# Performance work log

Measured on AMD Instinct MI355X. Metric: run time of the kernel, lower is better.

The kernel has to match this reference:

```python
import jax, jax.numpy as jnp
import numpy as np
from jax import lax

B, T, I, H = 256, 1024, 200, 16


def setup_inputs() -> dict:
    key = jax.random.key(0)
    ks = jax.random.split(key, 11)
    s = 0.05  # small init scale for weights
    return {
        "x": jax.random.normal(ks[0], (B, T, I), dtype=jnp.float32),
        "h0": jax.random.normal(ks[1], (B, H), dtype=jnp.float32),
        "c0": jax.random.normal(ks[2], (B, H), dtype=jnp.float32),
        "W_ih": jax.random.normal(ks[3], (4 * H, I), dtype=jnp.float32) * s,
        "W_hh": jax.random.normal(ks[4], (4 * H, H), dtype=jnp.float32) * s,
        "b_ih": jax.random.normal(ks[5], (4 * H,), dtype=jnp.float32) * s,
        "b_hh": jax.random.normal(ks[6], (4 * H,), dtype=jnp.float32) * s,
        "W1": jax.random.normal(ks[7], (H, H), dtype=jnp.float32) * s,
        "b1": jax.random.normal(ks[8], (H,), dtype=jnp.float32) * s,
        "W2": jax.random.normal(ks[9], (1, H), dtype=jnp.float32) * s,
        "b2": jax.random.normal(ks[10], (1,), dtype=jnp.float32) * s,
    }


def reference(x, h0, c0, W_ih, W_hh, b_ih, b_hh, W1, b1, W2, b2):
    # Precompute input projection for all timesteps: [B, T, 4H]
    x_proj = jnp.einsum("bti,gi->btg", x, W_ih) + b_ih + b_hh

    def step(carry, xt):  # xt: [B, 4H]
        h, c = carry
        gates = xt + h @ W_hh.T
        i, f, g, o = jnp.split(gates, 4, axis=-1)  # PyTorch gate order i,f,g,o
        i = jax.nn.sigmoid(i)
        f = jax.nn.sigmoid(f)
        g = jnp.tanh(g)
        o = jax.nn.sigmoid(o)
        c = f * c + i * g
        h = o * jnp.tanh(c)
        return (h, c), h

    _, hs = lax.scan(step, (h0, c0), x_proj.transpose(1, 0, 2))  # hs: [T, B, H]
    out = hs.transpose(1, 0, 2)  # [B, T, H]
    out = jax.nn.relu(out @ W1.T + b1)          # [B, T, H]
    out = jax.nn.sigmoid(out @ W2.T + b2)       # [B, T, 1]
    return jnp.mean(out, axis=1)                # [B, 1]
```

## Files before the change

kernel.cpp:

```cpp
#include <hip/hip_runtime.h>


#define T_LEN 1024
#define NB    256
#define CHUNK 128
#define NCH   (T_LEN / CHUNK)
#define XSTR  68

#define F2I(x) __float_as_int(x)
#define I2F(x) __int_as_float(x)
#define DPPF(v, ctrl) I2F(__builtin_amdgcn_update_dpp(F2I(v), F2I(v), (ctrl), 0xF, 0xF, false))
#define ROWSHL4(v) I2F(__builtin_amdgcn_update_dpp(F2I(v), F2I(v), 0x104, 0xF, 0xF, false))
#define RDLANE_I(v, l) __builtin_amdgcn_readlane((v), (l))

#define LOG2E 1.442695040888963f

typedef __bf16 bf16_t;
typedef bf16_t bf16x8 __attribute__((ext_vector_type(8)));
typedef float f32x4 __attribute__((ext_vector_type(4)));
typedef __fp16 half2_t __attribute__((ext_vector_type(2)));

#if __has_builtin(__builtin_amdgcn_exp2f)
__device__ __forceinline__ float fexp2(float x) { return __builtin_amdgcn_exp2f(x); }
#else
__device__ __forceinline__ float fexp2(float x) { return exp2f(x); }
#endif
#if __has_builtin(__builtin_amdgcn_rcpf)
__device__ __forceinline__ float frcp(float x) { return __builtin_amdgcn_rcpf(x); }
#else
__device__ __forceinline__ float frcp(float x) { return __fdividef(1.f, x); }
#endif

__device__ __forceinline__ half2_t i2h2(int x) { union { int i; half2_t h; } u; u.i = x; return u.h; }
__device__ __forceinline__ int h22i(half2_t h) { union { int i; half2_t h; } u; u.h = h; return u.i; }

#if __has_builtin(__builtin_amdgcn_fdot2)
#define FDOT2(a, b, c) __builtin_amdgcn_fdot2((a), (b), (c), false)
#else
__device__ __forceinline__ float FDOT2(half2_t a, half2_t b, float c) {
  return c + (float)a[0] * (float)b[0] + (float)a[1] * (float)b[1];
}
#endif

__device__ __forceinline__ float bf2f(unsigned short s) {
  return __uint_as_float(((unsigned int)s) << 16);
}
__device__ __forceinline__ unsigned int pkbf(float a, float b) {
  bf16_t x = (bf16_t)a, y = (bf16_t)b;
  unsigned short ux, uy;
  __builtin_memcpy(&ux, &x, 2); __builtin_memcpy(&uy, &y, 2);
  return (unsigned int)ux | ((unsigned int)uy << 16);
}

__global__ __launch_bounds__(256) void k0_prep(
    const float* __restrict__ Wih, const float* __restrict__ bih,
    const float* __restrict__ bhh, bf16x8* __restrict__ wB,
    float* __restrict__ biasPerm)
{
  const int idx = blockIdx.x * 256 + threadIdx.x;
  if (idx < 4 * 7 * 64) {
    const int f = idx / 448;
    const int rem = idx % 448;
    const int s = rem / 64;
    const int L = rem % 64;
    const int col = f * 16 + (L & 15);
    const int r = ((col & 3) << 4) | (col >> 2);
    const float sf = ((col & 3) == 2) ? (-2.f * LOG2E) : (-LOG2E);
    const int k0 = s * 32 + (L >> 4) * 8;
    bf16x8 v;
#pragma unroll
    for (int e = 0; e < 8; ++e) {
      const int k = k0 + e;
      const float w = (k < 200) ? (Wih[r * 200 + k] * sf) : 0.f;
      v[e] = (bf16_t)w;
    }
    wB[idx] = v;
  }
  if (blockIdx.x == 0 && threadIdx.x < 64) {
    const int c = threadIdx.x;
    const int r = ((c & 3) << 4) | (c >> 2);
    const float sf = ((c & 3) == 2) ? (-2.f * LOG2E) : (-LOG2E);
    biasPerm[c] = (bih[r] + bhh[r]) * sf;
  }
}

#define PACKH(hval, d0,d1,d2,d3,d4,d5,d6,d7) do {            \
    float _hn = ROWSHL4(hval);                               \
    int _pk = h22i(__builtin_amdgcn_cvt_pkrtz((hval), _hn)); \
    d0 = RDLANE_I(_pk,  0); d1 = RDLANE_I(_pk,  8);          \
    d2 = RDLANE_I(_pk, 16); d3 = RDLANE_I(_pk, 24);          \
    d4 = RDLANE_I(_pk, 32); d5 = RDLANE_I(_pk, 40);          \
    d6 = RDLANE_I(_pk, 48); d7 = RDLANE_I(_pk, 56);          \
  } while (0)

__global__ __launch_bounds__(256, 1) void mega(
    const float* __restrict__ x,
    const bf16x8* __restrict__ wB, const float* __restrict__ biasPerm,
    const float* __restrict__ h0, const float* __restrict__ c0,
    const float* __restrict__ Whh,
    unsigned short* __restrict__ hst)
{
  __shared__ float xsf[2][CHUNK * XSTR];

  const int tid  = threadIdx.x;
  const int lane = tid & 63;
  const int wid  = tid >> 6;
  const int b    = blockIdx.x;

  if (wid != 0) {
    const int pw   = wid - 1;
    const int L    = lane;
    const int mrow = L & 15;
    const int kg   = L >> 4;
    const int cb   = L & 15;

    bf16x8 Bv[28];
#pragma unroll
    for (int i = 0; i < 28; ++i) Bv[i] = wB[i * 64 + L];
    const float bv0 = biasPerm[ 0 + cb];
    const float bv1 = biasPerm[16 + cb];
    const float bv2 = biasPerm[32 + cb];
    const float bv3 = biasPerm[48 + cb];

    auto produce = [&](int pc) {
      for (int t8 = pw; t8 < 8; t8 += 3) {
        const int tile = pc * 8 + t8;
        const float* xr = x + ((size_t)b * T_LEN + tile * 16 + mrow) * 200;
        bf16x8 afr[7];
#pragma unroll
        for (int s = 0; s < 7; ++s) {
          const int k0 = s * 32 + kg * 8;
          bf16x8 v;
          if (k0 <= 192) {
            float4 a  = *reinterpret_cast<const float4*>(xr + k0);
            float4 b4 = *reinterpret_cast<const float4*>(xr + k0 + 4);
            v[0] = (bf16_t)a.x;  v[1] = (bf16_t)a.y;  v[2] = (bf16_t)a.z;  v[3] = (bf16_t)a.w;
            v[4] = (bf16_t)b4.x; v[5] = (bf16_t)b4.y; v[6] = (bf16_t)b4.z; v[7] = (bf16_t)b4.w;
          } else {
            v[0] = (bf16_t)0.f; v[1] = (bf16_t)0.f; v[2] = (bf16_t)0.f; v[3] = (bf16_t)0.f;
            v[4] = (bf16_t)0.f; v[5] = (bf16_t)0.f; v[6] = (bf16_t)0.f; v[7] = (bf16_t)0.f;
          }
          afr[s] = v;
        }

        f32x4 acc0 = {0.f,0.f,0.f,0.f}, acc1 = {0.f,0.f,0.f,0.f};
        f32x4 acc2 = {0.f,0.f,0.f,0.f}, acc3 = {0.f,0.f,0.f,0.f};
#pragma unroll
        for (int s = 0; s < 7; ++s) {
          acc0 = __builtin_amdgcn_mfma_f32_16x16x32_bf16(afr[s], Bv[0*7+s], acc0, 0,0,0);
          acc1 = __builtin_amdgcn_mfma_f32_16x16x32_bf16(afr[s], Bv[1*7+s], acc1, 0,0,0);
          acc2 = __builtin_amdgcn_mfma_f32_16x16x32_bf16(afr[s], Bv[2*7+s], acc2, 0,0,0);
          acc3 = __builtin_amdgcn_mfma_f32_16x16x32_bf16(afr[s], Bv[3*7+s], acc3, 0,0,0);
        }

        float* dst = xsf[pc & 1] + (t8 * 16) * XSTR;
#pragma unroll
        for (int q = 0; q < 4; ++q) {
          float* rowp = dst + (kg * 4 + q) * XSTR;
          rowp[ 0 + cb] = acc0[q] + bv0;
          rowp[16 + cb] = acc1[q] + bv1;
          rowp[32 + cb] = acc2[q] + bv2;
          rowp[48 + cb] = acc3[q] + bv3;
        }
      }
    };

    produce(0);
    for (int ch = 0; ch <= NCH; ++ch) {
      __syncthreads();
      if (ch + 1 < NCH) produce(ch + 1);
    }
    return;
  }

  __builtin_amdgcn_s_setprio(1);
  const int g = lane & 3;
  const int j = lane >> 2;
  const int r = (g << 4) | j;

  const float sfac = (g == 2) ? (-2.f * LOG2E) : (-LOG2E);
  const float pfac = (g == 0) ? (2.f * LOG2E) : ((g == 2) ? 2.f : 1.f);
  const float qfac = (g == 2) ? -1.f : 0.f;

  half2_t wpk[8];
#pragma unroll
  for (int q = 0; q < 4; ++q) {
    float4 w = *reinterpret_cast<const float4*>(Whh + r * 16 + q * 4);
    wpk[q * 2 + 0] = __builtin_amdgcn_cvt_pkrtz(w.x * sfac, w.y * sfac);
    wpk[q * 2 + 1] = __builtin_amdgcn_cvt_pkrtz(w.z * sfac, w.w * sfac);
  }

  float c = c0[b * 16 + j] * (2.f * LOG2E);
  float hmine = h0[b * 16 + j];
  int hp0, hp1, hp2, hp3, hp4, hp5, hp6, hp7;
  PACKH(hmine, hp0, hp1, hp2, hp3, hp4, hp5, hp6, hp7);

  unsigned short* hq = hst + (size_t)b * (16 * T_LEN) + j * T_LEN;

  __syncthreads();

  for (int ch = 0; ch < NCH; ++ch) {
    const float* xc = xsf[ch & 1];
    float buf[8];
#pragma unroll
    for (int u = 0; u < 8; ++u) buf[u] = xc[u * XSTR + lane];

    for (int ts = 0; ts < CHUNK; ts += 8) {
      float hsv[8];
#pragma unroll
      for (int u = 0; u < 8; ++u) {
        const float gin = buf[u];
        if (ts < CHUNK - 8) buf[u] = xc[(ts + 8 + u) * XSTR + lane];

        float d0 = FDOT2(wpk[0], i2h2(hp0), gin);
        d0 = FDOT2(wpk[1], i2h2(hp1), d0);
        d0 = FDOT2(wpk[2], i2h2(hp2), d0);
        d0 = FDOT2(wpk[3], i2h2(hp3), d0);
        float d1 = FDOT2(wpk[4], i2h2(hp4), 0.f);
        d1 = FDOT2(wpk[5], i2h2(hp5), d1);
        d1 = FDOT2(wpk[6], i2h2(hp6), d1);
        d1 = FDOT2(wpk[7], i2h2(hp7), d1);
        float pre = d0 + d1;

        float e = fexp2(pre);
        float z = frcp(1.f + e);
        float y = fmaf(pfac, z, qfac);

        float t1 = DPPF(y, 0x4E) * y;
        float ig = DPPF(t1, 0x00);
        c = fmaf(DPPF(y, 0x55), c, ig);

        float e2 = fexp2(c);
        float z2 = frcp(1.f + e2);
        float th = fmaf(-2.f, z2, 1.f);
        float h = DPPF(y, 0xFF) * th;

        PACKH(h, hp0, hp1, hp2, hp3, hp4, hp5, hp6, hp7);
        hsv[u] = h;
      }
      if (g == 0) {
        uint4 pk;
        pk.x = pkbf(hsv[0], hsv[1]);
        pk.y = pkbf(hsv[2], hsv[3]);
        pk.z = pkbf(hsv[4], hsv[5]);
        pk.w = pkbf(hsv[6], hsv[7]);
        *reinterpret_cast<uint4*>(hq + ch * CHUNK + ts) = pk;
      }
    }

    __syncthreads();
  }
}

__global__ __launch_bounds__(256) void k3_head(
    const unsigned short* __restrict__ hst,
    const float* __restrict__ W1, const float* __restrict__ b1,
    const float* __restrict__ W2, const float* __restrict__ b2,
    float* __restrict__ out)
{
  __shared__ float ws1[256];
  __shared__ float wsb1[16], wsw2[16];
  __shared__ float red[256];
  const int tid = threadIdx.x;
  const int b = blockIdx.x;

  ws1[tid] = W1[tid];
  if (tid < 16) { wsb1[tid] = b1[tid]; wsw2[tid] = W2[tid]; }
  __syncthreads();
  const float b2s = b2[0];

  const unsigned short* hb = hst + (size_t)b * (16 * T_LEN);
  float acc = 0.f;
#pragma unroll
  for (int it = 0; it < 2; ++it) {
    const int t2 = it * 256 + tid;
    unsigned int hp[16];
#pragma unroll
    for (int jj = 0; jj < 16; ++jj)
      hp[jj] = *reinterpret_cast<const unsigned int*>(hb + jj * T_LEN + 2 * t2);
    float h0v[16], h1v[16];
#pragma unroll
    for (int k = 0; k < 16; ++k) {
      h0v[k] = bf2f((unsigned short)(hp[k] & 0xffff));
      h1v[k] = bf2f((unsigned short)(hp[k] >> 16));
    }
    float s0 = b2s, s1 = b2s;
#pragma unroll
    for (int jj = 0; jj < 16; ++jj) {
      float p0 = wsb1[jj], p1 = wsb1[jj];
#pragma unroll
      for (int k = 0; k < 16; ++k) {
        const float wv = ws1[jj * 16 + k];
        p0 = fmaf(wv, h0v[k], p0);
        p1 = fmaf(wv, h1v[k], p1);
      }
      p0 = fmaxf(p0, 0.f);
      p1 = fmaxf(p1, 0.f);
      s0 = fmaf(wsw2[jj], p0, s0);
      s1 = fmaf(wsw2[jj], p1, s1);
    }
    acc += frcp(1.f + fexp2(-LOG2E * s0));
    acc += frcp(1.f + fexp2(-LOG2E * s1));
  }

  red[tid] = acc;
  __syncthreads();
  if (tid < 128) red[tid] += red[tid + 128];
  __syncthreads();
  if (tid < 64) {
    float v = red[tid] + red[tid + 64];
    v += __shfl_xor(v, 32, 64);
    v += __shfl_xor(v, 16, 64);
    v += __shfl_xor(v, 8, 64);
    v += __shfl_xor(v, 4, 64);
    v += __shfl_xor(v, 2, 64);
    v += __shfl_xor(v, 1, 64);
    if (tid == 0) out[b] = v * (1.f / T_LEN);
  }
}

extern "C" void kernel_launch(void* const* d_in, const int* in_sizes, int n_in,
                              void* d_out, int out_size, void* d_ws, size_t ws_size,
                              hipStream_t stream) {
  const float* x   = (const float*)d_in[0];
  const float* h0  = (const float*)d_in[1];
  const float* c0  = (const float*)d_in[2];
  const float* Wih = (const float*)d_in[3];
  const float* Whh = (const float*)d_in[4];
  const float* bih = (const float*)d_in[5];
  const float* bhh = (const float*)d_in[6];
  const float* W1  = (const float*)d_in[7];
  const float* b1  = (const float*)d_in[8];
  const float* W2  = (const float*)d_in[9];
  const float* b2  = (const float*)d_in[10];

  char* wsb = (char*)d_ws;
  unsigned short* hst = (unsigned short*)wsb;
  bf16x8* wB          = (bf16x8*)(wsb + 8388608);
  float* biasPerm     = (float*)(wsb + 8388608 + 32768);

  hipLaunchKernelGGL(k0_prep, dim3(7), dim3(256), 0, stream,
                     Wih, bih, bhh, wB, biasPerm);
  hipLaunchKernelGGL(mega, dim3(NB), dim3(256), 0, stream,
                     x, wB, biasPerm, h0, c0, Whh, hst);
  hipLaunchKernelGGL(k3_head, dim3(NB), dim3(256), 0, stream,
                     hst, W1, b1, W2, b2, (float*)d_out);
}
```

Baseline: 159.1 us.

## Fuse MLP head into recurrent kernel with hidden states kept in LDS

The head kernel is folded into the recurrent kernel. Hidden states now stay in a padded shared-memory buffer instead of going to global memory, and all 256 threads run the W1/W2 head and the reduction at the end of each block. This removes a kernel launch and the global round-trip of the hidden-state buffer. In exchange, producer warps now reload W_ih fragments from global or cache inside a non-unrolled loop instead of holding them in registers, LDS use grows, and the recurrence dot product is split into four partial chains.

```diff
diff --git a/kernel.cpp b/kernel.cpp
--- a/kernel.cpp
+++ b/kernel.cpp
@@ -6,6 +6,7 @@
 #define CHUNK 128
 #define NCH   (T_LEN / CHUNK)
 #define XSTR  68
+#define HSTR  1032
 
 #define F2I(x) __float_as_int(x)
 #define I2F(x) __int_as_float(x)
@@ -98,14 +99,24 @@
     const bf16x8* __restrict__ wB, const float* __restrict__ biasPerm,
     const float* __restrict__ h0, const float* __restrict__ c0,
     const float* __restrict__ Whh,
-    unsigned short* __restrict__ hst)
+    const float* __restrict__ W1, const float* __restrict__ b1,
+    const float* __restrict__ W2, const float* __restrict__ b2,
+    float* __restrict__ out)
 {
   __shared__ float xsf[2][CHUNK * XSTR];
+  __shared__ __attribute__((aligned(16))) unsigned short hstL[16 * HSTR];
+  __shared__ float ws1[256];
+  __shared__ float wsb1[16], wsw2[16];
+  __shared__ float red[256];
 
   const int tid  = threadIdx.x;
   const int lane = tid & 63;
   const int wid  = tid >> 6;
   const int b    = blockIdx.x;
+
+  ws1[tid] = W1[tid];
+  if (tid < 16) { wsb1[tid] = b1[tid]; wsw2[tid] = W2[tid]; }
+  const float b2s = b2[0];
 
   if (wid != 0) {
     const int pw   = wid - 1;
@@ -114,9 +125,6 @@
     const int kg   = L >> 4;
     const int cb   = L & 15;
 
-    bf16x8 Bv[28];
-#pragma unroll
-    for (int i = 0; i < 28; ++i) Bv[i] = wB[i * 64 + L];
     const float bv0 = biasPerm[ 0 + cb];
     const float bv1 = biasPerm[16 + cb];
     const float bv2 = biasPerm[32 + cb];
@@ -145,12 +153,16 @@
 
         f32x4 acc0 = {0.f,0.f,0.f,0.f}, acc1 = {0.f,0.f,0.f,0.f};
         f32x4 acc2 = {0.f,0.f,0.f,0.f}, acc3 = {0.f,0.f,0.f,0.f};
-#pragma unroll
+#pragma unroll 1
         for (int s = 0; s < 7; ++s) {
-          acc0 = __builtin_amdgcn_mfma_f32_16x16x32_bf16(afr[s], Bv[0*7+s], acc0, 0,0,0);
-          acc1 = __builtin_amdgcn_mfma_f32_16x16x32_bf16(afr[s], Bv[1*7+s], acc1, 0,0,0);
-          acc2 = __builtin_amdgcn_mfma_f32_16x16x32_bf16(afr[s], Bv[2*7+s], acc2, 0,0,0);
-          acc3 = __builtin_amdgcn_mfma_f32_16x16x32_bf16(afr[s], Bv[3*7+s], acc3, 0,0,0);
+          const bf16x8 B0 = wB[(0 * 7 + s) * 64 + L];
+          const bf16x8 B1 = wB[(1 * 7 + s) * 64 + L];
+          const bf16x8 B2 = wB[(2 * 7 + s) * 64 + L];
+          const bf16x8 B3 = wB[(3 * 7 + s) * 64 + L];
+          acc0 = __builtin_amdgcn_mfma_f32_16x16x32_bf16(afr[s], B0, acc0, 0,0,0);
+          acc1 = __builtin_amdgcn_mfma_f32_16x16x32_bf16(afr[s], B1, acc1, 0,0,0);
+          acc2 = __builtin_amdgcn_mfma_f32_16x16x32_bf16(afr[s], B2, acc2, 0,0,0);
+          acc3 = __builtin_amdgcn_mfma_f32_16x16x32_bf16(afr[s], B3, acc3, 0,0,0);
         }
 
         float* dst = xsf[pc & 1] + (t8 * 16) * XSTR;
@@ -166,141 +178,109 @@
     };
 
     produce(0);
-    for (int ch = 0; ch <= NCH; ++ch) {
+    for (int ch = 0; ch < NCH; ++ch) {
       __syncthreads();
       if (ch + 1 < NCH) produce(ch + 1);
     }
-    return;
-  }
-
-  __builtin_amdgcn_s_setprio(1);
-  const int g = lane & 3;
-  const int j = lane >> 2;
-  const int r = (g << 4) | j;
-
-  const float sfac = (g == 2) ? (-2.f * LOG2E) : (-LOG2E);
-  const float pfac = (g == 0) ? (2.f * LOG2E) : ((g == 2) ? 2.f : 1.f);
-  const float qfac = (g == 2) ? -1.f : 0.f;
-
-  half2_t wpk[8];
-#pragma unroll
-  for (int q = 0; q < 4; ++q) {
-    float4 w = *reinterpret_cast<const float4*>(Whh + r * 16 + q * 4);
-    wpk[q * 2 + 0] = __builtin_amdgcn_cvt_pkrtz(w.x * sfac, w.y * sfac);
-    wpk[q * 2 + 1] = __builtin_amdgcn_cvt_pkrtz(w.z * sfac, w.w * sfac);
-  }
-
-  float c = c0[b * 16 + j] * (2.f * LOG2E);
-  float hmine = h0[b * 16 + j];
-  int hp0, hp1, hp2, hp3, hp4, hp5, hp6, hp7;
-  PACKH(hmine, hp0, hp1, hp2, hp3, hp4, hp5, hp6, hp7);
-
-  unsigned short* hq = hst + (size_t)b * (16 * T_LEN) + j * T_LEN;
-
-  __syncthreads();
-
-  for (int ch = 0; ch < NCH; ++ch) {
-    const float* xc = xsf[ch & 1];
-    float buf[8];
-#pragma unroll
-    for (int u = 0; u < 8; ++u) buf[u] = xc[u * XSTR + lane];
-
-    for (int ts = 0; ts < CHUNK; ts += 8) {
-      float hsv[8];
-#pragma unroll
-      for (int u = 0; u < 8; ++u) {
-        const float gin = buf[u];
-        if (ts < CHUNK - 8) buf[u] = xc[(ts + 8 + u) * XSTR + lane];
-
-        float d0 = FDOT2(wpk[0], i2h2(hp0), gin);
-        d0 = FDOT2(wpk[1], i2h2(hp1), d0);
-        d0 = FDOT2(wpk[2], i2h2(hp2), d0);
-        d0 = FDOT2(wpk[3], i2h2(hp3), d0);
-        float d1 = FDOT2(wpk[4], i2h2(hp4), 0.f);
-        d1 = FDOT2(wpk[5], i2h2(hp5), d1);
-        d1 = FDOT2(wpk[6], i2h2(hp6), d1);
-        d1 = FDOT2(wpk[7], i2h2(hp7), d1);
-        float pre = d0 + d1;
-
-        float e = fexp2(pre);
-        float z = frcp(1.f + e);
-        float y = fmaf(pfac, z, qfac);
-
-        float t1 = DPPF(y, 0x4E) * y;
-        float ig = DPPF(t1, 0x00);
-        c = fmaf(DPPF(y, 0x55), c, ig);
-
-        float e2 = fexp2(c);
-        float z2 = frcp(1.f + e2);
-        float th = fmaf(-2.f, z2, 1.f);
-        float h = DPPF(y, 0xFF) * th;
-
-        PACKH(h, hp0, hp1, hp2, hp3, hp4, hp5, hp6, hp7);
-        hsv[u] = h;
+    __syncthreads();
+  } else {
+    __builtin_amdgcn_s_setprio(1);
+    const int g = lane & 3;
+    const int j = lane >> 2;
+    const int r = (g << 4) | j;
+
+    const float sfac = (g == 2) ? (-2.f * LOG2E) : (-LOG2E);
+    const float pfac = (g == 0) ? (2.f * LOG2E) : ((g == 2) ? 2.f : 1.f);
+    const float qfac = (g == 2) ? -1.f : 0.f;
+
+    half2_t wpk[8];
+#pragma unroll
+    for (int q = 0; q < 4; ++q) {
+      float4 w = *reinterpret_cast<const float4*>(Whh + r * 16 + q * 4);
+      wpk[q * 2 + 0] = __builtin_amdgcn_cvt_pkrtz(w.x * sfac, w.y * sfac);
+      wpk[q * 2 + 1] = __builtin_amdgcn_cvt_pkrtz(w.z * sfac, w.w * sfac);
+    }
+
+    float c = c0[b * 16 + j] * (2.f * LOG2E);
+    float hmine = h0[b * 16 + j];
+    int hp0, hp1, hp2, hp3, hp4, hp5, hp6, hp7;
+    PACKH(hmine, hp0, hp1, hp2, hp3, hp4, hp5, hp6, hp7);
+
+    __syncthreads();
+
+    for (int ch = 0; ch < NCH; ++ch) {
+      const float* xc = xsf[ch & 1];
+      float buf[8];
+#pragma unroll
+      for (int u = 0; u < 8; ++u) buf[u] = xc[u * XSTR + lane];
+
+      for (int ts = 0; ts < CHUNK; ts += 8) {
+        float hsv[8];
+#pragma unroll
+        for (int u = 0; u < 8; ++u) {
+          const float gin = buf[u];
+          int tn = ts + 8 + u;
+          tn = (tn < CHUNK) ? tn : (CHUNK - 1);
+          buf[u] = xc[tn * XSTR + lane];
+
+          float e0 = FDOT2(wpk[0], i2h2(hp0), gin);
+          e0 = FDOT2(wpk[1], i2h2(hp1), e0);
+          float e1 = FDOT2(wpk[2], i2h2(hp2), 0.f);
+          e1 = FDOT2(wpk[3], i2h2(hp3), e1);
+          float e2 = FDOT2(wpk[4], i2h2(hp4), 0.f);
+          e2 = FDOT2(wpk[5], i2h2(hp5), e2);
+          float e3 = FDOT2(wpk[6], i2h2(hp6), 0.f);
+          e3 = FDOT2(wpk[7], i2h2(hp7), e3);
+          float pre = (e0 + e1) + (e2 + e3);
+
+          float e = fexp2(pre);
+          float z = frcp(1.f + e);
+          float y = fmaf(pfac, z, qfac);
+
+          float t1 = DPPF(y, 0x4E) * y;
+          float ig = DPPF(t1, 0x00);
+          c = fmaf(DPPF(y, 0x55), c, ig);
+
+          float e2x = fexp2(c);
+          float z2 = frcp(1.f + e2x);
+          float th = fmaf(-2.f, z2, 1.f);
+          float h = DPPF(y, 0xFF) * th;
+
+          PACKH(h, hp0, hp1, hp2, hp3, hp4, hp5, hp6, hp7);
+          hsv[u] = h;
+        }
+        if (g == 0) {
+          uint4 pk;
+          pk.x = pkbf(hsv[0], hsv[1]);
+          pk.y = pkbf(hsv[2], hsv[3]);
+          pk.z = pkbf(hsv[4], hsv[5]);
+          pk.w = pkbf(hsv[6], hsv[7]);
+          *reinterpret_cast<uint4*>(&hstL[j * HSTR + ch * CHUNK + ts]) = pk;
+        }
       }
-      if (g == 0) {
-        uint4 pk;
-        pk.x = pkbf(hsv[0], hsv[1]);
-        pk.y = pkbf(hsv[2], hsv[3]);
-        pk.z = pkbf(hsv[4], hsv[5]);
-        pk.w = pkbf(hsv[6], hsv[7]);
-        *reinterpret_cast<uint4*>(hq + ch * CHUNK + ts) = pk;
-      }
-    }
-
-    __syncthreads();
-  }
-}
-
-__global__ __launch_bounds__(256) void k3_head(
-    const unsigned short* __restrict__ hst,
-    const float* __restrict__ W1, const float* __restrict__ b1,
-    const float* __restrict__ W2, const float* __restrict__ b2,
-    float* __restrict__ out)
-{
-  __shared__ float ws1[256];
-  __shared__ float wsb1[16], wsw2[16];
-  __shared__ float red[256];
-  const int tid = threadIdx.x;
-  const int b = blockIdx.x;
-
-  ws1[tid] = W1[tid];
-  if (tid < 16) { wsb1[tid] = b1[tid]; wsw2[tid] = W2[tid]; }
-  __syncthreads();
-  const float b2s = b2[0];
-
-  const unsigned short* hb = hst + (size_t)b * (16 * T_LEN);
+
+      __syncthreads();
+    }
+  }
+
   float acc = 0.f;
 #pragma unroll
-  for (int it = 0; it < 2; ++it) {
-    const int t2 = it * 256 + tid;
-    unsigned int hp[16];
+  for (int it = 0; it < 4; ++it) {
+    const int t = it * 256 + tid;
+    float h[16];
 #pragma unroll
     for (int jj = 0; jj < 16; ++jj)
-      hp[jj] = *reinterpret_cast<const unsigned int*>(hb + jj * T_LEN + 2 * t2);
-    float h0v[16], h1v[16];
-#pragma unroll
-    for (int k = 0; k < 16; ++k) {
-      h0v[k] = bf2f((unsigned short)(hp[k] & 0xffff));
-      h1v[k] = bf2f((unsigned short)(hp[k] >> 16));
-    }
-    float s0 = b2s, s1 = b2s;
+      h[jj] = bf2f(hstL[jj * HSTR + t]);
+    float s = b2s;
 #pragma unroll
     for (int jj = 0; jj < 16; ++jj) {
-      float p0 = wsb1[jj], p1 = wsb1[jj];
-#pragma unroll
-      for (int k = 0; k < 16; ++k) {
-        const float wv = ws1[jj * 16 + k];
-        p0 = fmaf(wv, h0v[k], p0);
-        p1 = fmaf(wv, h1v[k], p1);
-      }
-      p0 = fmaxf(p0, 0.f);
-      p1 = fmaxf(p1, 0.f);
-      s0 = fmaf(wsw2[jj], p0, s0);
-      s1 = fmaf(wsw2[jj], p1, s1);
-    }
-    acc += frcp(1.f + fexp2(-LOG2E * s0));
-    acc += frcp(1.f + fexp2(-LOG2E * s1));
+      float p = wsb1[jj];
+#pragma unroll
+      for (int k = 0; k < 16; ++k) p = fmaf(ws1[jj * 16 + k], h[k], p);
+      p = fmaxf(p, 0.f);
+      s = fmaf(wsw2[jj], p, s);
+    }
+    acc += frcp(1.f + fexp2(-LOG2E * s));
   }
 
   red[tid] = acc;
@@ -335,14 +315,11 @@
   const float* b2  = (const float*)d_in[10];
 
   char* wsb = (char*)d_ws;
-  unsigned short* hst = (unsigned short*)wsb;
-  bf16x8* wB          = (bf16x8*)(wsb + 8388608);
-  float* biasPerm     = (float*)(wsb + 8388608 + 32768);
+  bf16x8* wB      = (bf16x8*)wsb;
+  float* biasPerm = (float*)(wsb + 32768);
 
   hipLaunchKernelGGL(k0_prep, dim3(7), dim3(256), 0, stream,
                      Wih, bih, bhh, wB, biasPerm);
   hipLaunchKernelGGL(mega, dim3(NB), dim3(256), 0, stream,
-                     x, wB, biasPerm, h0, c0, Whh, hst);
-  hipLaunchKernelGGL(k3_head, dim3(NB), dim3(256), 0, stream,
-                     hst, W1, b1, W2, b2, (float*)d_out);
-}
+                     x, wB, biasPerm, h0, c0, Whh, W1, b1, W2, b2, (float*)d_out);
+}
```

Result: slower. 457.2 us (+187.4%).

## Store gate projections as bf16 in LDS, stage weights via global_load_lds

Applied to the files above, without the earlier changes.

The projected gate inputs are now stored in LDS as bf16 with the log2e/sign scaling applied at write time, instead of fp32 with a padded stride. The W_ih fragments are DMA'd into shared memory with global_load_lds rather than held in 28 registers per producer wave, and the recurrent dot product is split into four independent partial sums to shorten its dependency chain. Prefetch of the next chunk's first inputs moves to after the barrier, and the sync count changes so producers and consumer stay matched. In exchange the input projections lose precision to bf16, and each MFMA now reads its B operand from LDS.

```diff
diff --git a/kernel.cpp b/kernel.cpp
--- a/kernel.cpp
+++ b/kernel.cpp
@@ -5,12 +5,11 @@
 #define NB    256
 #define CHUNK 128
 #define NCH   (T_LEN / CHUNK)
-#define XSTR  68
 
 #define F2I(x) __float_as_int(x)
 #define I2F(x) __int_as_float(x)
+#define ROWSHL4(v) I2F(__builtin_amdgcn_update_dpp(F2I(v), F2I(v), 0x104, 0xF, 0xF, false))
 #define DPPF(v, ctrl) I2F(__builtin_amdgcn_update_dpp(F2I(v), F2I(v), (ctrl), 0xF, 0xF, false))
-#define ROWSHL4(v) I2F(__builtin_amdgcn_update_dpp(F2I(v), F2I(v), 0x104, 0xF, 0xF, false))
 #define RDLANE_I(v, l) __builtin_amdgcn_readlane((v), (l))
 
 #define LOG2E 1.442695040888963f
@@ -65,13 +64,12 @@
     const int L = rem % 64;
     const int col = f * 16 + (L & 15);
     const int r = ((col & 3) << 4) | (col >> 2);
-    const float sf = ((col & 3) == 2) ? (-2.f * LOG2E) : (-LOG2E);
     const int k0 = s * 32 + (L >> 4) * 8;
     bf16x8 v;
 #pragma unroll
     for (int e = 0; e < 8; ++e) {
       const int k = k0 + e;
-      const float w = (k < 200) ? (Wih[r * 200 + k] * sf) : 0.f;
+      const float w = (k < 200) ? Wih[r * 200 + k] : 0.f;
       v[e] = (bf16_t)w;
     }
     wB[idx] = v;
@@ -79,8 +77,7 @@
   if (blockIdx.x == 0 && threadIdx.x < 64) {
     const int c = threadIdx.x;
     const int r = ((c & 3) << 4) | (c >> 2);
-    const float sf = ((c & 3) == 2) ? (-2.f * LOG2E) : (-LOG2E);
-    biasPerm[c] = (bih[r] + bhh[r]) * sf;
+    biasPerm[c] = bih[r] + bhh[r];
   }
 }
 
@@ -100,7 +97,8 @@
     const float* __restrict__ Whh,
     unsigned short* __restrict__ hst)
 {
-  __shared__ float xsf[2][CHUNK * XSTR];
+  __shared__ unsigned short xs[2][CHUNK * 64];
+  __shared__ bf16x8 Bs[28 * 64];
 
   const int tid  = threadIdx.x;
   const int lane = tid & 63;
@@ -114,13 +112,22 @@
     const int kg   = L >> 4;
     const int cb   = L & 15;
 
-    bf16x8 Bv[28];
-#pragma unroll
-    for (int i = 0; i < 28; ++i) Bv[i] = wB[i * 64 + L];
+    {
+      const unsigned short* src = (const unsigned short*)wB;
+      unsigned short* dst = (unsigned short*)Bs;
+      for (int it = pw; it < 28; it += 3) {
+        __builtin_amdgcn_global_load_lds(
+            (const __attribute__((address_space(1))) unsigned int*)(src + it * 512 + L * 8),
+            (__attribute__((address_space(3))) unsigned int*)(dst + it * 512),
+            16, 0, 0);
+      }
+    }
+
     const float bv0 = biasPerm[ 0 + cb];
     const float bv1 = biasPerm[16 + cb];
     const float bv2 = biasPerm[32 + cb];
     const float bv3 = biasPerm[48 + cb];
+    const float cs  = ((cb & 3) == 2) ? (-2.f * LOG2E) : (-LOG2E);
 
     auto produce = [&](int pc) {
       for (int t8 = pw; t8 < 8; t8 += 3) {
@@ -147,29 +154,31 @@
         f32x4 acc2 = {0.f,0.f,0.f,0.f}, acc3 = {0.f,0.f,0.f,0.f};
 #pragma unroll
         for (int s = 0; s < 7; ++s) {
-          acc0 = __builtin_amdgcn_mfma_f32_16x16x32_bf16(afr[s], Bv[0*7+s], acc0, 0,0,0);
-          acc1 = __builtin_amdgcn_mfma_f32_16x16x32_bf16(afr[s], Bv[1*7+s], acc1, 0,0,0);
-          acc2 = __builtin_amdgcn_mfma_f32_16x16x32_bf16(afr[s], Bv[2*7+s], acc2, 0,0,0);
-          acc3 = __builtin_amdgcn_mfma_f32_16x16x32_bf16(afr[s], Bv[3*7+s], acc3, 0,0,0);
+          acc0 = __builtin_amdgcn_mfma_f32_16x16x32_bf16(afr[s], Bs[(0*7+s)*64 + L], acc0, 0,0,0);
+          acc1 = __builtin_amdgcn_mfma_f32_16x16x32_bf16(afr[s], Bs[(1*7+s)*64 + L], acc1, 0,0,0);
+          acc2 = __builtin_amdgcn_mfma_f32_16x16x32_bf16(afr[s], Bs[(2*7+s)*64 + L], acc2, 0,0,0);
+          acc3 = __builtin_amdgcn_mfma_f32_16x16x32_bf16(afr[s], Bs[(3*7+s)*64 + L], acc3, 0,0,0);
         }
 
-        float* dst = xsf[pc & 1] + (t8 * 16) * XSTR;
+        __bf16* dst = (__bf16*)&xs[pc & 1][(t8 * 16) * 64];
 #pragma unroll
         for (int q = 0; q < 4; ++q) {
-          float* rowp = dst + (kg * 4 + q) * XSTR;
-          rowp[ 0 + cb] = acc0[q] + bv0;
-          rowp[16 + cb] = acc1[q] + bv1;
-          rowp[32 + cb] = acc2[q] + bv2;
-          rowp[48 + cb] = acc3[q] + bv3;
+          __bf16* rowp = dst + (kg * 4 + q) * 64;
+          rowp[ 0 + cb] = (bf16_t)((acc0[q] + bv0) * cs);
+          rowp[16 + cb] = (bf16_t)((acc1[q] + bv1) * cs);
+          rowp[32 + cb] = (bf16_t)((acc2[q] + bv2) * cs);
+          rowp[48 + cb] = (bf16_t)((acc3[q] + bv3) * cs);
         }
       }
     };
 
+    __syncthreads();
     produce(0);
-    for (int ch = 0; ch <= NCH; ++ch) {
+    for (int ch = 0; ch < NCH; ++ch) {
       __syncthreads();
       if (ch + 1 < NCH) produce(ch + 1);
     }
+    __syncthreads();
     return;
   }
 
@@ -198,29 +207,34 @@
   unsigned short* hq = hst + (size_t)b * (16 * T_LEN) + j * T_LEN;
 
   __syncthreads();
+  __syncthreads();
+
+  float buf[8];
+#pragma unroll
+  for (int u = 0; u < 8; ++u)
+    buf[u] = bf2f(xs[0][u * 64 + lane]);
 
   for (int ch = 0; ch < NCH; ++ch) {
-    const float* xc = xsf[ch & 1];
-    float buf[8];
-#pragma unroll
-    for (int u = 0; u < 8; ++u) buf[u] = xc[u * XSTR + lane];
+    const unsigned short* xcur = xs[ch & 1];
 
     for (int ts = 0; ts < CHUNK; ts += 8) {
       float hsv[8];
 #pragma unroll
       for (int u = 0; u < 8; ++u) {
         const float gin = buf[u];
-        if (ts < CHUNK - 8) buf[u] = xc[(ts + 8 + u) * XSTR + lane];
-
-        float d0 = FDOT2(wpk[0], i2h2(hp0), gin);
-        d0 = FDOT2(wpk[1], i2h2(hp1), d0);
-        d0 = FDOT2(wpk[2], i2h2(hp2), d0);
-        d0 = FDOT2(wpk[3], i2h2(hp3), d0);
-        float d1 = FDOT2(wpk[4], i2h2(hp4), 0.f);
-        d1 = FDOT2(wpk[5], i2h2(hp5), d1);
-        d1 = FDOT2(wpk[6], i2h2(hp6), d1);
-        d1 = FDOT2(wpk[7], i2h2(hp7), d1);
-        float pre = d0 + d1;
+        int tn = ts + 8 + u;
+        tn = (tn < CHUNK) ? tn : (CHUNK - 1);
+        buf[u] = bf2f(xcur[tn * 64 + lane]);
+
+        float e0 = FDOT2(wpk[0], i2h2(hp0), gin);
+        e0 = FDOT2(wpk[1], i2h2(hp1), e0);
+        float e1 = FDOT2(wpk[2], i2h2(hp2), 0.f);
+        e1 = FDOT2(wpk[3], i2h2(hp3), e1);
+        float e2 = FDOT2(wpk[4], i2h2(hp4), 0.f);
+        e2 = FDOT2(wpk[5], i2h2(hp5), e2);
+        float e3 = FDOT2(wpk[6], i2h2(hp6), 0.f);
+        e3 = FDOT2(wpk[7], i2h2(hp7), e3);
+        float pre = (e0 + e1) + (e2 + e3);
 
         float e = fexp2(pre);
         float z = frcp(1.f + e);
@@ -230,8 +244,8 @@
         float ig = DPPF(t1, 0x00);
         c = fmaf(DPPF(y, 0x55), c, ig);
 
-        float e2 = fexp2(c);
-        float z2 = frcp(1.f + e2);
+        float e2x = fexp2(c);
+        float z2 = frcp(1.f + e2x);
         float th = fmaf(-2.f, z2, 1.f);
         float h = DPPF(y, 0xFF) * th;
 
@@ -249,6 +263,11 @@
     }
 
     __syncthreads();
+    if (ch + 1 < NCH) {
+      const unsigned short* xn = xs[(ch + 1) & 1];
+#pragma unroll
+      for (int u = 0; u < 8; ++u) buf[u] = bf2f(xn[u * 64 + lane]);
+    }
   }
 }
 
```

After: 134.3 us. 1.18x faster.
